# Kernel optimization log

Hardware: AMD Instinct MI355X
Metric: run time of the kernel (lower is better)

## Reference

```python
import jax, jax.numpy as jnp
import numpy as np

N_NODES = 50000
N_EDGES = 600000
F_IN = 128
HID = 128
N_CLASSES = 10


def _gcn_graph(edge_index, n_nodes):
    # PyG GCNConv: add self-loops, deg computed on target (col) with weight 1,
    # norm_e = deg^-1/2[src] * deg^-1/2[dst]
    src = jnp.concatenate([edge_index[0], jnp.arange(n_nodes, dtype=edge_index.dtype)])
    dst = jnp.concatenate([edge_index[1], jnp.arange(n_nodes, dtype=edge_index.dtype)])
    deg = jax.ops.segment_sum(jnp.ones_like(dst, dtype=jnp.float32), dst, num_segments=n_nodes)
    dinv = jnp.where(deg > 0, jax.lax.rsqrt(deg), 0.0)
    norm = dinv[src] * dinv[dst]  # [E+N]
    return src, dst, norm


def _gcn_layer(x, W, b, src, dst, norm, n_nodes):
    h = x @ W                      # [N, out] linear first (bias applied post-agg)
    m = h[src] * norm[:, None]     # gather + scale, [E+N, out]
    out = jax.ops.segment_sum(m, dst, num_segments=n_nodes)  # scatter-add
    return out + b


def setup_inputs() -> dict:
    key = jax.random.key(0)
    ks = jax.random.split(key, 4)
    x = jax.random.normal(ks[0], (N_NODES, F_IN), dtype=jnp.float32)
    edge_index = jax.random.randint(ks[1], (2, N_EDGES), 0, N_NODES, dtype=jnp.int64)
    # Glorot-ish init scale for weights
    W_stack = jax.random.normal(ks[2], (8, HID, HID), dtype=jnp.float32) * (1.0 / np.sqrt(HID))
    b_stack = jnp.zeros((8, HID), dtype=jnp.float32)
    W_out = jax.random.normal(ks[3], (HID, N_CLASSES), dtype=jnp.float32) * (1.0 / np.sqrt(HID))
    b_out = jnp.zeros((N_CLASSES,), dtype=jnp.float32)
    return {"x": x, "edge_index": edge_index, "W_stack": W_stack, "b_stack": b_stack,
            "W_out": W_out, "b_out": b_out}


def reference(x, edge_index, W_stack, b_stack, W_out, b_out):
    n_nodes = x.shape[0]
    src, dst, norm = _gcn_graph(edge_index, n_nodes)
    h = x
    for i in range(8):  # conv1..conv8 with ELU
        h = jax.nn.elu(_gcn_layer(h, W_stack[i], b_stack[i], src, dst, norm, n_nodes))
    # conv9: no activation
    return _gcn_layer(h, W_out, b_out, src, dst, norm, n_nodes)
```

## Files before the change

### kernel.cpp

```cpp
#include <hip/hip_runtime.h>
#include <math.h>

#define NN 50000
#define NE 600000
#define HID 128
#define NCLS 10
#define T2S 16

typedef __bf16 bf16x8 __attribute__((ext_vector_type(8)));
typedef float f32x16 __attribute__((ext_vector_type(16)));

__device__ __forceinline__ void split3(float f, ushort& h, ushort& m, ushort& l) {
    unsigned uh = __float_as_uint(f) & 0xffff0000u;
    float fm = f - __uint_as_float(uh);
    unsigned um = __float_as_uint(fm) & 0xffff0000u;
    float fl = fm - __uint_as_float(um);
    h = (ushort)(uh >> 16);
    m = (ushort)(um >> 16);
    l = (ushort)(__float_as_uint(fl) >> 16);
}


__global__ __launch_bounds__(256) void k_count(const int* __restrict__ edge,
                                               int* __restrict__ counts) {
    int e = blockIdx.x * 256 + threadIdx.x;
    if (e < NE) atomicAdd(&counts[edge[NE + e]], 1);
}

__device__ __forceinline__ int wave_incl_scan(int x, int lane) {
#pragma unroll
    for (int off = 1; off < 64; off <<= 1) {
        int y = __shfl_up(x, off, 64);
        if (lane >= off) x += y;
    }
    return x;
}

__global__ __launch_bounds__(256) void k_scan1(const int* __restrict__ counts,
                                               int* __restrict__ rowptr,
                                               int* __restrict__ bsum,
                                               float* __restrict__ dinv) {
    __shared__ int ws[4];
    int tid = threadIdx.x;
    int i = blockIdx.x * 256 + tid;
    int lane = tid & 63, wv = tid >> 6;
    int v = (i < NN) ? counts[i] : 0;
    if (i < NN) dinv[i] = rsqrtf((float)(v + 1));
    int x = wave_incl_scan(v, lane);
    if (lane == 63) ws[wv] = x;
    __syncthreads();
    int off = 0;
    for (int j = 0; j < wv; ++j) off += ws[j];
    if (i < NN) rowptr[i] = off + x - v;
    if (tid == 255) bsum[blockIdx.x] = off + x;
}

__global__ __launch_bounds__(256) void k_scan2(int* __restrict__ bsum, int n) {
    __shared__ int ws[4];
    int tid = threadIdx.x;
    int lane = tid & 63, wv = tid >> 6;
    int v = (tid < n) ? bsum[tid] : 0;
    int x = wave_incl_scan(v, lane);
    if (lane == 63) ws[wv] = x;
    __syncthreads();
    int off = 0;
    for (int j = 0; j < wv; ++j) off += ws[j];
    __syncthreads();
    if (tid < n) bsum[tid] = off + x - v;
}

__global__ __launch_bounds__(256) void k_scan3(int* __restrict__ rowptr,
                                               const int* __restrict__ bsum) {
    int i = blockIdx.x * 256 + threadIdx.x;
    if (i < NN) rowptr[i] += bsum[blockIdx.x];
    if (i == 0) rowptr[NN] = NE;
}

__global__ __launch_bounds__(256) void k_fill(const int* __restrict__ edge,
                                              const int* __restrict__ rowptr,
                                              int* __restrict__ cursor,
                                              const float* __restrict__ dinv,
                                              int2* __restrict__ csr) {
    int e = blockIdx.x * 256 + threadIdx.x;
    if (e >= NE) return;
    int s = edge[e], d = edge[NE + e];
    int slot = atomicSub(&cursor[d], 1) - 1;
    csr[rowptr[d] + slot] = make_int2(s, __float_as_int(dinv[s] * dinv[d]));
}


__global__ __launch_bounds__(256) void k_split_w(const float* __restrict__ Wst,
                                                 ushort* __restrict__ Wt3) {
    int i = blockIdx.x * 256 + threadIdx.x;
    if (i >= 8 * HID * HID) return;
    int l = i >> 14;
    int k = (i >> 7) & 127;
    int n = i & 127;
    ushort h, m, lo;
    split3(Wst[i], h, m, lo);
    size_t base = (size_t)l * 3 * HID * HID + (size_t)n * HID + k;
    Wt3[base] = h;
    Wt3[base + HID * HID] = m;
    Wt3[base + 2 * HID * HID] = lo;
}


__global__ __launch_bounds__(256) void k_mfma_gemm(const float* __restrict__ H,
                                                   const ushort* __restrict__ Wt,
                                                   float* __restrict__ T) {
    __shared__ ushort As[3][128][40];
    __shared__ ushort Bs[3][128][40];
    int tid = threadIdx.x;
    int lane = tid & 63, w = tid >> 6;
    int wy = w >> 1, wx = w & 1;
    int l31 = lane & 31, lh = lane >> 5;
    int rowbase = blockIdx.x * 128;

    int arow = tid >> 1;
    int kh = (tid & 1) * 16;
    int garow = rowbase + arow;
    if (garow >= NN) garow = NN - 1;
    size_t aoff = (size_t)garow * HID;

    f32x16 acc[2][2] = {};

    float4 af0, af1, af2, af3;
    {
        const float4* asrc = (const float4*)(H + aoff + kh);
        af0 = asrc[0]; af1 = asrc[1]; af2 = asrc[2]; af3 = asrc[3];
    }
    uint4 rb[6];
#pragma unroll
    for (int c = 0; c < 6; ++c) {
        int chunk = c * 256 + tid;
        int p = chunk >> 9;
        int rem = chunk & 511;
        int col = rem >> 2;
        int q = rem & 3;
        rb[c] = *(const uint4*)(Wt + p * (HID * HID) + col * HID + q * 8);
    }

    for (int k0 = 0; k0 < HID; k0 += 32) {
        float av[16] = {af0.x, af0.y, af0.z, af0.w, af1.x, af1.y, af1.z, af1.w,
                        af2.x, af2.y, af2.z, af2.w, af3.x, af3.y, af3.z, af3.w};
        union { ushort u[16]; uint4 v[2]; } ph, pm, pl;
#pragma unroll
        for (int q = 0; q < 16; ++q) split3(av[q], ph.u[q], pm.u[q], pl.u[q]);

        __syncthreads();
        *(uint4*)&As[0][arow][kh] = ph.v[0];
        *(uint4*)&As[0][arow][kh + 8] = ph.v[1];
        *(uint4*)&As[1][arow][kh] = pm.v[0];
        *(uint4*)&As[1][arow][kh + 8] = pm.v[1];
        *(uint4*)&As[2][arow][kh] = pl.v[0];
        *(uint4*)&As[2][arow][kh + 8] = pl.v[1];
#pragma unroll
        for (int c = 0; c < 6; ++c) {
            int chunk = c * 256 + tid;
            int p = chunk >> 9;
            int rem = chunk & 511;
            int col = rem >> 2;
            int q = rem & 3;
            *(uint4*)&Bs[p][col][q * 8] = rb[c];
        }
        __syncthreads();

        int k0n = k0 + 32;
        if (k0n < HID) {
            const float4* asrc = (const float4*)(H + aoff + k0n + kh);
            af0 = asrc[0]; af1 = asrc[1]; af2 = asrc[2]; af3 = asrc[3];
#pragma unroll
            for (int c = 0; c < 6; ++c) {
                int chunk = c * 256 + tid;
                int p = chunk >> 9;
                int rem = chunk & 511;
                int col = rem >> 2;
                int q = rem & 3;
                rb[c] = *(const uint4*)(Wt + p * (HID * HID) + col * HID + k0n + q * 8);
            }
        }

#pragma unroll
        for (int ks = 0; ks < 32; ks += 16) {
            int kk = ks + lh * 8;
            bf16x8 a[3][2], b[3][2];
#pragma unroll
            for (int p = 0; p < 3; ++p)
#pragma unroll
                for (int h = 0; h < 2; ++h) {
                    a[p][h] = *(const bf16x8*)&As[p][wy * 64 + h * 32 + l31][kk];
                    b[p][h] = *(const bf16x8*)&Bs[p][wx * 64 + h * 32 + l31][kk];
                }
#pragma unroll
            for (int h = 0; h < 2; ++h)
#pragma unroll
                for (int c = 0; c < 2; ++c)
                    acc[h][c] = __builtin_amdgcn_mfma_f32_32x32x16_bf16(a[0][h], b[0][c], acc[h][c], 0, 0, 0);
#pragma unroll
            for (int h = 0; h < 2; ++h)
#pragma unroll
                for (int c = 0; c < 2; ++c)
                    acc[h][c] = __builtin_amdgcn_mfma_f32_32x32x16_bf16(a[0][h], b[1][c], acc[h][c], 0, 0, 0);
#pragma unroll
            for (int h = 0; h < 2; ++h)
#pragma unroll
                for (int c = 0; c < 2; ++c)
                    acc[h][c] = __builtin_amdgcn_mfma_f32_32x32x16_bf16(a[1][h], b[0][c], acc[h][c], 0, 0, 0);
#pragma unroll
            for (int h = 0; h < 2; ++h)
#pragma unroll
                for (int c = 0; c < 2; ++c)
                    acc[h][c] = __builtin_amdgcn_mfma_f32_32x32x16_bf16(a[0][h], b[2][c], acc[h][c], 0, 0, 0);
#pragma unroll
            for (int h = 0; h < 2; ++h)
#pragma unroll
                for (int c = 0; c < 2; ++c)
                    acc[h][c] = __builtin_amdgcn_mfma_f32_32x32x16_bf16(a[1][h], b[1][c], acc[h][c], 0, 0, 0);
#pragma unroll
            for (int h = 0; h < 2; ++h)
#pragma unroll
                for (int c = 0; c < 2; ++c)
                    acc[h][c] = __builtin_amdgcn_mfma_f32_32x32x16_bf16(a[2][h], b[0][c], acc[h][c], 0, 0, 0);
        }
    }
#pragma unroll
    for (int h = 0; h < 2; ++h)
#pragma unroll
        for (int c = 0; c < 2; ++c)
#pragma unroll
            for (int reg = 0; reg < 16; ++reg) {
                int r = (reg & 3) + 8 * (reg >> 2) + 4 * lh;
                int gr = rowbase + wy * 64 + h * 32 + r;
                if (gr < NN)
                    T[(size_t)gr * HID + wx * 64 + c * 32 + l31] = acc[h][c][reg];
            }
}


__global__ __launch_bounds__(256) void k_gather_agg(const float* __restrict__ T,
                                                    float* __restrict__ Hout,
                                                    const int* __restrict__ rowptr,
                                                    const int2* __restrict__ csr,
                                                    const float* __restrict__ dinv,
                                                    const float* __restrict__ bias) {
    int lane = threadIdx.x & 63;
    int node = (blockIdx.x * 256 + threadIdx.x) >> 6;
    if (node >= NN) return;
    int slot = lane >> 5, l31 = lane & 31;

    int beg = rowptr[node], end = rowptr[node + 1];
    float sn = dinv[node];

    float4 acc = {0.f, 0.f, 0.f, 0.f};
    if (slot == 1) {
        float4 tv = ((const float4*)(T + (size_t)node * HID))[l31];
        float4 bv = ((const float4*)bias)[l31];
        float s2 = sn * sn;
        acc.x = s2 * tv.x + bv.x;
        acc.y = s2 * tv.y + bv.y;
        acc.z = s2 * tv.z + bv.z;
        acc.w = s2 * tv.w + bv.w;
    }

    const int2 zed = make_int2(0, 0);
    int p = beg + slot;
    int2 e0 = (p < end) ? csr[p] : zed;
    int2 e1 = (p + 2 < end) ? csr[p + 2] : zed;
    int2 e2 = (p + 4 < end) ? csr[p + 4] : zed;
    int2 e3 = (p + 6 < end) ? csr[p + 6] : zed;
    for (; p < end; p += 8) {
        float4 u0 = ((const float4*)(T + (size_t)e0.x * HID))[l31];
        float4 u1 = ((const float4*)(T + (size_t)e1.x * HID))[l31];
        float4 u2 = ((const float4*)(T + (size_t)e2.x * HID))[l31];
        float4 u3 = ((const float4*)(T + (size_t)e3.x * HID))[l31];
        float w0 = __int_as_float(e0.y), w1 = __int_as_float(e1.y);
        float w2 = __int_as_float(e2.y), w3 = __int_as_float(e3.y);
        e0 = (p + 8 < end) ? csr[p + 8] : zed;
        e1 = (p + 10 < end) ? csr[p + 10] : zed;
        e2 = (p + 12 < end) ? csr[p + 12] : zed;
        e3 = (p + 14 < end) ? csr[p + 14] : zed;
        acc.x += w0 * u0.x; acc.y += w0 * u0.y; acc.z += w0 * u0.z; acc.w += w0 * u0.w;
        acc.x += w1 * u1.x; acc.y += w1 * u1.y; acc.z += w1 * u1.z; acc.w += w1 * u1.w;
        acc.x += w2 * u2.x; acc.y += w2 * u2.y; acc.z += w2 * u2.z; acc.w += w2 * u2.w;
        acc.x += w3 * u3.x; acc.y += w3 * u3.y; acc.z += w3 * u3.z; acc.w += w3 * u3.w;
    }

    acc.x += __shfl_xor(acc.x, 32, 64);
    acc.y += __shfl_xor(acc.y, 32, 64);
    acc.z += __shfl_xor(acc.z, 32, 64);
    acc.w += __shfl_xor(acc.w, 32, 64);

    if (slot == 0) {
        float4 r = acc;
        r.x = r.x > 0.f ? r.x : expm1f(r.x);
        r.y = r.y > 0.f ? r.y : expm1f(r.y);
        r.z = r.z > 0.f ? r.z : expm1f(r.z);
        r.w = r.w > 0.f ? r.w : expm1f(r.w);
        ((float4*)(Hout + (size_t)node * HID))[l31] = r;
    }
}


__global__ __launch_bounds__(256) void k_matmul_out(const float* __restrict__ H,
                                                    const float* __restrict__ W,
                                                    float* __restrict__ T2) {
    __shared__ float Ws[128 * 11];
    int tid = threadIdx.x;
    for (int m = tid; m < HID * NCLS; m += 256) {
        int k = m / NCLS, c = m - k * NCLS;
        Ws[k * 11 + c] = W[m];
    }
    __syncthreads();
    int row = (blockIdx.x * 256 + tid) >> 4;
    int c16 = tid & 15;
    if (row >= NN) return;
    const float4* h4 = (const float4*)(H + (size_t)row * HID) + c16 * 2;
    float4 h0 = h4[0], h1 = h4[1];
    float hv[8] = {h0.x, h0.y, h0.z, h0.w, h1.x, h1.y, h1.z, h1.w};
    float acc[NCLS];
#pragma unroll
    for (int c = 0; c < NCLS; ++c) acc[c] = 0.f;
#pragma unroll
    for (int j = 0; j < 8; ++j) {
        const float* wr = &Ws[(c16 * 8 + j) * 11];
#pragma unroll
        for (int c = 0; c < NCLS; ++c) acc[c] += hv[j] * wr[c];
    }
#pragma unroll
    for (int off = 8; off >= 1; off >>= 1) {
#pragma unroll
        for (int c = 0; c < NCLS; ++c) acc[c] += __shfl_xor(acc[c], off, 16);
    }
    if (c16 < NCLS) T2[(size_t)row * T2S + c16] = acc[c16];
}

__global__ __launch_bounds__(256) void k_gather_out(const float* __restrict__ T2,
                                                    float* __restrict__ out,
                                                    const int* __restrict__ rowptr,
                                                    const int2* __restrict__ csr,
                                                    const float* __restrict__ dinv,
                                                    const float* __restrict__ bias) {
    int lane = threadIdx.x & 63;
    int node = (blockIdx.x * 256 + threadIdx.x) >> 6;
    if (node >= NN) return;
    int slot = lane >> 4, c = lane & 15;
    int beg = rowptr[node], end = rowptr[node + 1];
    float acc = 0.f;
    if (c < NCLS) {
        for (int i = beg + slot; i < end; i += 4) {
            int2 e = csr[i];
            acc += __int_as_float(e.y) * T2[(size_t)e.x * T2S + c];
        }
    }
    acc += __shfl_xor(acc, 16, 64);
    acc += __shfl_xor(acc, 32, 64);
    if (slot == 0 && c < NCLS) {
        float sn = dinv[node];
        sn *= sn;
        out[node * NCLS + c] = acc + sn * T2[(size_t)node * T2S + c] + bias[c];
    }
}


extern "C" void kernel_launch(void* const* d_in, const int* in_sizes, int n_in,
                              void* d_out, int out_size, void* d_ws, size_t ws_size,
                              hipStream_t stream) {
    (void)in_sizes; (void)n_in; (void)out_size; (void)ws_size;
    const float* x       = (const float*)d_in[0];
    const int*   edge    = (const int*)d_in[1];
    const float* W_stack = (const float*)d_in[2];
    const float* b_stack = (const float*)d_in[3];
    const float* W_out   = (const float*)d_in[4];
    const float* b_out   = (const float*)d_in[5];
    float* out = (float*)d_out;

    char* ws = (char*)d_ws;
    const size_t bigbuf = (size_t)NN * HID * sizeof(float);
    float* X      = (float*)ws;
    float* Y      = (float*)(ws + bigbuf);
    char*  p      = ws + 2 * bigbuf;
    int2*  csr    = (int2*)p;              p += sizeof(int2) * NE;
    float* dinv   = (float*)p;             p += sizeof(float) * NN;
    int*   rowptr = (int*)p;               p += sizeof(int) * (NN + 1);
    int*   counts = (int*)p;               p += sizeof(int) * NN;
    int*   bsum   = (int*)p;               p += sizeof(int) * 256;
    p = (char*)(((size_t)p + 15) & ~(size_t)15);
    ushort* Wt3 = (ushort*)p;  p += sizeof(ushort) * 8 * 3 * HID * HID;

    const int NB_N  = (NN + 255) / 256;
    const int NB_E  = (NE + 255) / 256;
    const int NB_G  = (NN + 127) / 128;
    const int NB_A  = (NN * 64 + 255) / 256;
    const int NB_W  = (NN * 64 + 255) / 256;
    const int NB_O  = (NN * 16 + 255) / 256;
    const int NB_SW = (8 * HID * HID + 255) / 256;

    hipMemsetAsync(counts, 0, sizeof(int) * NN, stream);
    k_count<<<NB_E, 256, 0, stream>>>(edge, counts);
    k_scan1<<<NB_N, 256, 0, stream>>>(counts, rowptr, bsum, dinv);
    k_scan2<<<1, 256, 0, stream>>>(bsum, NB_N);
    k_scan3<<<NB_N, 256, 0, stream>>>(rowptr, bsum);
    k_fill<<<NB_E, 256, 0, stream>>>(edge, rowptr, counts, dinv, csr);

    k_split_w<<<NB_SW, 256, 0, stream>>>(W_stack, Wt3);

    const float* Hin = x;
    for (int l = 0; l < 8; ++l) {
        k_mfma_gemm<<<NB_G, 256, 0, stream>>>(Hin, Wt3 + (size_t)l * 3 * HID * HID, Y);
        k_gather_agg<<<NB_A, 256, 0, stream>>>(Y, X, rowptr, csr, dinv,
                                               b_stack + (size_t)l * HID);
        Hin = X;
    }

    k_matmul_out<<<NB_O, 256, 0, stream>>>(X, W_out, Y);
    k_gather_out<<<NB_W, 256, 0, stream>>>(Y, out, rowptr, csr, dinv, b_out);
}
```

Measured before the change: 800.1 us.

## Pre-swizzle split weights into MFMA fragment layout and load B directly to registers

Weight planes are now stored in a k-blocked [plane][k/16][n][16] layout so each lane can fetch its bf16x8 MFMA B fragment straight from global memory (L2-resident) into registers. The B shared-memory tile and its staging stores are removed, which cuts LDS traffic and LDS footprint. The register double-buffering of A and B prefetch is dropped, so global load latency is now exposed within each k-step. Redundant per-wave global reads of the same weight fragments also increase.

```diff
diff --git a/kernel.cpp b/kernel.cpp
--- a/kernel.cpp
+++ b/kernel.cpp
@@ -90,7 +90,7 @@
 
 
 __global__ __launch_bounds__(256) void k_split_w(const float* __restrict__ Wst,
-                                                 ushort* __restrict__ Wt3) {
+                                                 ushort* __restrict__ Wt4) {
     int i = blockIdx.x * 256 + threadIdx.x;
     if (i >= 8 * HID * HID) return;
     int l = i >> 14;
@@ -98,10 +98,12 @@
     int n = i & 127;
     ushort h, m, lo;
     split3(Wst[i], h, m, lo);
-    size_t base = (size_t)l * 3 * HID * HID + (size_t)n * HID + k;
-    Wt3[base] = h;
-    Wt3[base + HID * HID] = m;
-    Wt3[base + 2 * HID * HID] = lo;
+    int ks = k >> 4, r = k & 15;
+    size_t base = ((((size_t)l * 3) * 8 + ks) * 128 + n) * 16 + r;
+    const size_t pstride = (size_t)8 * 128 * 16;
+    Wt4[base] = h;
+    Wt4[base + pstride] = m;
+    Wt4[base + 2 * pstride] = lo;
 }
 
 
@@ -109,7 +111,6 @@
                                                    const ushort* __restrict__ Wt,
                                                    float* __restrict__ T) {
     __shared__ ushort As[3][128][40];
-    __shared__ ushort Bs[3][128][40];
     int tid = threadIdx.x;
     int lane = tid & 63, w = tid >> 6;
     int wy = w >> 1, wx = w & 1;
@@ -122,25 +123,24 @@
     if (garow >= NN) garow = NN - 1;
     size_t aoff = (size_t)garow * HID;
 
+    const ushort* wbase = Wt + ((size_t)wx * 64 + l31) * 16 + lh * 8;
+
     f32x16 acc[2][2] = {};
 
-    float4 af0, af1, af2, af3;
-    {
-        const float4* asrc = (const float4*)(H + aoff + kh);
-        af0 = asrc[0]; af1 = asrc[1]; af2 = asrc[2]; af3 = asrc[3];
-    }
-    uint4 rb[6];
-#pragma unroll
-    for (int c = 0; c < 6; ++c) {
-        int chunk = c * 256 + tid;
-        int p = chunk >> 9;
-        int rem = chunk & 511;
-        int col = rem >> 2;
-        int q = rem & 3;
-        rb[c] = *(const uint4*)(Wt + p * (HID * HID) + col * HID + q * 8);
-    }
-
     for (int k0 = 0; k0 < HID; k0 += 32) {
+        int ks0 = k0 >> 4;
+        uint4 bf[2][3][2];
+#pragma unroll
+        for (int s = 0; s < 2; ++s)
+#pragma unroll
+            for (int p = 0; p < 3; ++p)
+#pragma unroll
+                for (int c = 0; c < 2; ++c)
+                    bf[s][p][c] = *(const uint4*)(wbase +
+                        (((size_t)p * 8 + ks0 + s) * 128 + c * 32) * 16);
+
+        const float4* asrc = (const float4*)(H + aoff + k0 + kh);
+        float4 af0 = asrc[0], af1 = asrc[1], af2 = asrc[2], af3 = asrc[3];
         float av[16] = {af0.x, af0.y, af0.z, af0.w, af1.x, af1.y, af1.z, af1.w,
                         af2.x, af2.y, af2.z, af2.w, af3.x, af3.y, af3.z, af3.w};
         union { ushort u[16]; uint4 v[2]; } ph, pm, pl;
@@ -154,43 +154,21 @@
         *(uint4*)&As[1][arow][kh + 8] = pm.v[1];
         *(uint4*)&As[2][arow][kh] = pl.v[0];
         *(uint4*)&As[2][arow][kh + 8] = pl.v[1];
-#pragma unroll
-        for (int c = 0; c < 6; ++c) {
-            int chunk = c * 256 + tid;
-            int p = chunk >> 9;
-            int rem = chunk & 511;
-            int col = rem >> 2;
-            int q = rem & 3;
-            *(uint4*)&Bs[p][col][q * 8] = rb[c];
-        }
         __syncthreads();
 
-        int k0n = k0 + 32;
-        if (k0n < HID) {
-            const float4* asrc = (const float4*)(H + aoff + k0n + kh);
-            af0 = asrc[0]; af1 = asrc[1]; af2 = asrc[2]; af3 = asrc[3];
-#pragma unroll
-            for (int c = 0; c < 6; ++c) {
-                int chunk = c * 256 + tid;
-                int p = chunk >> 9;
-                int rem = chunk & 511;
-                int col = rem >> 2;
-                int q = rem & 3;
-                rb[c] = *(const uint4*)(Wt + p * (HID * HID) + col * HID + k0n + q * 8);
+#pragma unroll
+        for (int s = 0; s < 2; ++s) {
+            int kk = s * 16 + lh * 8;
+            bf16x8 a[3][2], b[3][2];
+#pragma unroll
+            for (int p = 0; p < 3; ++p) {
+#pragma unroll
+                for (int h = 0; h < 2; ++h)
+                    a[p][h] = *(const bf16x8*)&As[p][wy * 64 + h * 32 + l31][kk];
+#pragma unroll
+                for (int c = 0; c < 2; ++c)
+                    b[p][c] = *(const bf16x8*)&bf[s][p][c];
             }
-        }
-
-#pragma unroll
-        for (int ks = 0; ks < 32; ks += 16) {
-            int kk = ks + lh * 8;
-            bf16x8 a[3][2], b[3][2];
-#pragma unroll
-            for (int p = 0; p < 3; ++p)
-#pragma unroll
-                for (int h = 0; h < 2; ++h) {
-                    a[p][h] = *(const bf16x8*)&As[p][wy * 64 + h * 32 + l31][kk];
-                    b[p][h] = *(const bf16x8*)&Bs[p][wx * 64 + h * 32 + l31][kk];
-                }
 #pragma unroll
             for (int h = 0; h < 2; ++h)
 #pragma unroll
@@ -385,7 +363,7 @@
     int*   counts = (int*)p;               p += sizeof(int) * NN;
     int*   bsum   = (int*)p;               p += sizeof(int) * 256;
     p = (char*)(((size_t)p + 15) & ~(size_t)15);
-    ushort* Wt3 = (ushort*)p;  p += sizeof(ushort) * 8 * 3 * HID * HID;
+    ushort* Wt4 = (ushort*)p;  p += sizeof(ushort) * 8 * 3 * HID * HID;
 
     const int NB_N  = (NN + 255) / 256;
     const int NB_E  = (NE + 255) / 256;
@@ -402,11 +380,11 @@
     k_scan3<<<NB_N, 256, 0, stream>>>(rowptr, bsum);
     k_fill<<<NB_E, 256, 0, stream>>>(edge, rowptr, counts, dinv, csr);
 
-    k_split_w<<<NB_SW, 256, 0, stream>>>(W_stack, Wt3);
+    k_split_w<<<NB_SW, 256, 0, stream>>>(W_stack, Wt4);
 
     const float* Hin = x;
     for (int l = 0; l < 8; ++l) {
-        k_mfma_gemm<<<NB_G, 256, 0, stream>>>(Hin, Wt3 + (size_t)l * 3 * HID * HID, Y);
+        k_mfma_gemm<<<NB_G, 256, 0, stream>>>(Hin, Wt4 + (size_t)l * 3 * HID * HID, Y);
         k_gather_agg<<<NB_A, 256, 0, stream>>>(Y, X, rowptr, csr, dinv,
                                                b_stack + (size_t)l * HID);
         Hin = X;
```

After: 708.3 us. 11.5% less time.
